# Optimization experiments

Hardware: AMD Instinct MI355X
Metric: run time of the kernel (lower is better)

## Reference

```python
import jax, jax.numpy as jnp
import numpy as np

B, C, H, W = 16, 512, 32, 32
HW = H * W  # == input_features == output_features for shapes to be consistent


def setup_inputs() -> dict:
    key = jax.random.key(0)
    k1, k2, k3 = jax.random.split(key, 3)
    node1 = jax.random.normal(k1, (B, C, H, W), dtype=jnp.float32)
    node2 = jax.random.normal(k2, (B, C, H, W), dtype=jnp.float32)
    # nn.Linear(input_features, output_features, bias=False).weight: [out, in]
    W_c = jax.random.normal(k3, (HW, HW), dtype=jnp.float32) * (1.0 / np.sqrt(HW))
    return {"node1": node1, "node2": node2, "W_c": W_c}


def reference(node1, node2, W_c):
    b, c, h, w = node1.shape
    hw = h * w
    n1 = node1.reshape(b, c, hw)  # [B, C, HW]
    n2 = node2.reshape(b, c, hw)  # [B, C, HW]
    # x = W_c(n1): Linear applies y = x @ W^T  -> [B, C, HW_out]
    x = jnp.einsum('bch,oh->bco', n1, W_c)
    # e = bmm(x.permute(0,2,1), n2): [B, HW_out, C] @ [B, C, HW] -> [B, HW_out, HW]
    e = jnp.einsum('bco,bch->boh', x, n2)
    a = jax.nn.softmax(e, axis=-1)  # softmax over last dim (HW of node2)
    # m = bmm(n2, a): [B, C, HW] @ [B, HW, HW] -> [B, C, HW]
    m = jnp.einsum('bck,bkj->bcj', n2, a)
    return m
```

## Files before the change

### kernel.cpp

```cpp
#include <hip/hip_runtime.h>
#include <math.h>


typedef _Float16 f16;
typedef _Float16 f16x8 __attribute__((ext_vector_type(8)));
typedef _Float16 f16x4 __attribute__((ext_vector_type(4)));
typedef float f32x4 __attribute__((ext_vector_type(4)));

__device__ __forceinline__ void glds16(const void* g, void* l) {
    __builtin_amdgcn_global_load_lds((const __attribute__((address_space(1))) void*)g,
                                     (__attribute__((address_space(3))) void*)l, 16, 0, 0);
}

__global__ __launch_bounds__(256) void prep(const float* __restrict__ n1,
                                            const float* __restrict__ Wc,
                                            const float* __restrict__ n2,
                                            f16* __restrict__ n1f, f16* __restrict__ Wf,
                                            f16* __restrict__ n2f, f16* __restrict__ n2t) {
    const int bid = blockIdx.x, tid = threadIdx.x;
    if (bid < 4608) {
        const float* s = (bid < 4096) ? n1 : Wc;
        f16* d = (bid < 4096) ? n1f : Wf;
        const size_t i = ((size_t)(bid < 4096 ? bid : bid - 4096) * 256 + tid) * 8;
        f32x4 a = *(const f32x4*)(s + i);
        f32x4 b = *(const f32x4*)(s + i + 4);
        f16x8 o;
        o[0] = (f16)a[0]; o[1] = (f16)a[1]; o[2] = (f16)a[2]; o[3] = (f16)a[3];
        o[4] = (f16)b[0]; o[5] = (f16)b[1]; o[6] = (f16)b[2]; o[7] = (f16)b[3];
        *(f16x8*)(d + i) = o;
        return;
    }
    const int id = bid - 4608;
    const int b = id >> 7;
    const int ry = (id & 127) >> 4;
    const int cx = id & 15;
    const float* S = n2 + (size_t)b * 512 * 1024;
    f16* Dn = n2f + (size_t)b * 512 * 1024;
    f16* Dt = n2t + (size_t)b * 1024 * 512;
    __shared__ f16 Ts[64 * 72];
    const int r0 = ry * 64, c0 = cx * 64;
    const int rr = tid >> 3, cc8 = (tid & 7) * 8;
#pragma unroll
    for (int h = 0; h < 2; ++h) {
        const int row = r0 + rr + 32 * h;
        const float* s = S + (size_t)row * 1024 + c0 + cc8;
        f32x4 a = *(const f32x4*)s, bq = *(const f32x4*)(s + 4);
        f16x8 o;
        o[0] = (f16)a[0]; o[1] = (f16)a[1]; o[2] = (f16)a[2]; o[3] = (f16)a[3];
        o[4] = (f16)bq[0]; o[5] = (f16)bq[1]; o[6] = (f16)bq[2]; o[7] = (f16)bq[3];
        *(f16x8*)&Ts[(rr + 32 * h) * 72 + cc8] = o;
        *(f16x8*)(Dn + (size_t)row * 1024 + c0 + cc8) = o;
    }
    __syncthreads();
    const int j = tid >> 2, k16 = (tid & 3) * 16;
    f16* d = Dt + (size_t)(c0 + j) * 512 + r0 + k16;
    f16x8 o0, o1;
#pragma unroll
    for (int i = 0; i < 8; ++i) {
        o0[i] = Ts[(k16 + i) * 72 + j];
        o1[i] = Ts[(k16 + 8 + i) * 72 + j];
    }
    *(f16x8*)d = o0;
    *(f16x8*)(d + 8) = o1;
}

__global__ __launch_bounds__(256) void softmax_stats(const f16* __restrict__ E,
                                                     float* __restrict__ Mg,
                                                     float* __restrict__ Si) {
    const int wave = threadIdx.x >> 6, lane = threadIdx.x & 63;
    const int row = blockIdx.x * 4 + wave;
    const f16* p = E + (size_t)row * 1024 + lane * 16;
    f16x8 a = *(const f16x8*)p, b = *(const f16x8*)(p + 8);
    float v[16];
#pragma unroll
    for (int i = 0; i < 8; ++i) { v[i] = (float)a[i]; v[i + 8] = (float)b[i]; }
    float m = v[0];
#pragma unroll
    for (int i = 1; i < 16; ++i) m = fmaxf(m, v[i]);
#pragma unroll
    for (int off = 1; off < 64; off <<= 1) m = fmaxf(m, __shfl_xor(m, off, 64));
    float s = 0.f;
#pragma unroll
    for (int i = 0; i < 16; ++i) s += __expf(v[i] - m);
#pragma unroll
    for (int off = 1; off < 64; off <<= 1) s += __shfl_xor(s, off, 64);
    if (lane == 0) { Mg[row] = m; Si[row] = 1.0f / s; }
}

__global__ __launch_bounds__(256) void tr_scale(const f16* __restrict__ S,
                                                const float* __restrict__ Mg,
                                                const float* __restrict__ Si,
                                                f16* __restrict__ D) {
    const int b = blockIdx.z;
    S += (size_t)b * 1024 * 1024;
    D += (size_t)b * 1024 * 1024;
    __shared__ f16 Ts[64 * 72];
    const int r0 = blockIdx.y * 64, c0 = blockIdx.x * 64;
    const int tid = threadIdx.x;
    const int rr = tid >> 3, cc8 = (tid & 7) * 8;
#pragma unroll
    for (int h = 0; h < 2; ++h) {
        const int row = r0 + rr + 32 * h;
        const float mg = Mg[b * 1024 + row];
        const float si = Si[b * 1024 + row];
        f16x8 v = *(const f16x8*)(S + (size_t)row * 1024 + c0 + cc8);
        f16x8 o;
#pragma unroll
        for (int i = 0; i < 8; ++i) o[i] = (f16)(__expf((float)v[i] - mg) * si);
        *(f16x8*)&Ts[(rr + 32 * h) * 72 + cc8] = o;
    }
    __syncthreads();
    const int j = tid >> 2, k16 = (tid & 3) * 16;
    f16* d = D + (size_t)(c0 + j) * 1024 + r0 + k16;
    f16x8 o0, o1;
#pragma unroll
    for (int i = 0; i < 8; ++i) {
        o0[i] = Ts[(k16 + i) * 72 + j];
        o1[i] = Ts[(k16 + 8 + i) * 72 + j];
    }
    *(f16x8*)d = o0;
    *(f16x8*)(d + 8) = o1;
}

__global__ __launch_bounds__(512) void gemm1_nt_xt(const f16* __restrict__ A,
                                                   const f16* __restrict__ Bw,
                                                   f16* __restrict__ Xt) {
    const int M = 512, K = 1024;
    const int id = blockIdx.x;
    const int xcd = id & 7, loc = id >> 3;
    const int b = xcd * 2 + (loc >> 5);
    const int m0 = ((loc >> 3) & 3) * 128;
    const int n0 = (loc & 7) * 128;
    A += (size_t)b * M * K;
    Xt += (size_t)b * 1024 * M;
    __shared__ __attribute__((aligned(16))) f16 SM[128 * 136];
    f16* As = SM;
    f16* Bs = SM + 4096;
    const int tid = threadIdx.x, lane = tid & 63, wave = tid >> 6;
    const int col = lane & 15, quad = lane >> 4;
    const int wm = (wave & 1) * 64, wn = (wave >> 1) * 32;
    const int off = wave * 1024 + lane * 16;
    const char* gA = (const char*)(A + (size_t)(m0 + (off >> 6)) * K) + (off & 63);
    const char* gB = (const char*)(Bw + (size_t)(n0 + (off >> 6)) * K) + (off & 63);
    char* lA = (char*)As + wave * 1024;
    char* lB = (char*)Bs + wave * 1024;

    f32x4 acc[4][2] = {};
    for (int kb = 0; kb < K * 2; kb += 64) {
        glds16(gA + kb, lA);
        glds16(gB + kb, lB);
        __syncthreads();
        f16x8 fa[4], fb[2];
#pragma unroll
        for (int u = 0; u < 4; ++u) fa[u] = *(const f16x8*)&As[(wm + u * 16 + col) * 32 + quad * 8];
#pragma unroll
        for (int v = 0; v < 2; ++v) fb[v] = *(const f16x8*)&Bs[(wn + v * 16 + col) * 32 + quad * 8];
#pragma unroll
        for (int u = 0; u < 4; ++u)
#pragma unroll
            for (int v = 0; v < 2; ++v)
                acc[u][v] = __builtin_amdgcn_mfma_f32_16x16x32_f16(fa[u], fb[v], acc[u][v], 0, 0, 0);
        __syncthreads();
    }
    f16* Tt = SM;
#pragma unroll
    for (int u = 0; u < 4; ++u)
#pragma unroll
        for (int v = 0; v < 2; ++v) {
            f16x4 p;
#pragma unroll
            for (int r = 0; r < 4; ++r) p[r] = (f16)acc[u][v][r];
            *(f16x4*)&Tt[(wn + v * 16 + col) * 136 + wm + u * 16 + quad * 4] = p;
        }
    __syncthreads();
    const int j = tid >> 2, seg = (tid & 3) * 32;
    f16* dst = Xt + (size_t)(n0 + j) * M + m0 + seg;
#pragma unroll
    for (int c8 = 0; c8 < 32; c8 += 8)
        *(f16x8*)(dst + c8) = *(const f16x8*)&Tt[j * 136 + seg + c8];
}

__global__ __launch_bounds__(512) void gemm2_nt_e(const f16* __restrict__ A,
                                                  const f16* __restrict__ B,
                                                  f16* __restrict__ E) {
    const int K = 512;
    const int id = blockIdx.x;
    const int xcd = id & 7, loc = id >> 3;
    const int b = xcd * 2 + (loc >> 6);
    const int m0 = ((loc >> 3) & 7) * 128;
    const int n0 = (loc & 7) * 128;
    A += (size_t)b * 1024 * K;
    B += (size_t)b * 1024 * K;
    E += (size_t)b * 1024 * 1024;
    __shared__ __attribute__((aligned(16))) f16 As[128 * 32], Bs[128 * 32];
    const int tid = threadIdx.x, lane = tid & 63, wave = tid >> 6;
    const int col = lane & 15, quad = lane >> 4;
    const int wm = (wave & 1) * 64, wn = (wave >> 1) * 32;
    const int off = wave * 1024 + lane * 16;
    const char* gA = (const char*)(A + (size_t)(m0 + (off >> 6)) * K) + (off & 63);
    const char* gB = (const char*)(B + (size_t)(n0 + (off >> 6)) * K) + (off & 63);
    char* lA = (char*)As + wave * 1024;
    char* lB = (char*)Bs + wave * 1024;

    f32x4 acc[4][2] = {};
    for (int kb = 0; kb < K * 2; kb += 64) {
        glds16(gA + kb, lA);
        glds16(gB + kb, lB);
        __syncthreads();
        f16x8 fa[4], fb[2];
#pragma unroll
        for (int u = 0; u < 4; ++u) fa[u] = *(const f16x8*)&As[(wm + u * 16 + col) * 32 + quad * 8];
#pragma unroll
        for (int v = 0; v < 2; ++v) fb[v] = *(const f16x8*)&Bs[(wn + v * 16 + col) * 32 + quad * 8];
#pragma unroll
        for (int u = 0; u < 4; ++u)
#pragma unroll
            for (int v = 0; v < 2; ++v)
                acc[u][v] = __builtin_amdgcn_mfma_f32_16x16x32_f16(fa[u], fb[v], acc[u][v], 0, 0, 0);
        __syncthreads();
    }
#pragma unroll
    for (int u = 0; u < 4; ++u)
#pragma unroll
        for (int v = 0; v < 2; ++v)
#pragma unroll
            for (int r = 0; r < 4; ++r)
                E[(size_t)(m0 + wm + u * 16 + quad * 4 + r) * 1024 + n0 + wn + v * 16 + col] =
                    (f16)acc[u][v][r];
}

__global__ __launch_bounds__(512) void gemm3_nt_out(const f16* __restrict__ A,
                                                    const f16* __restrict__ Bt,
                                                    float* __restrict__ C) {
    const int K = 1024;
    const int id = blockIdx.x;
    const int xcd = id & 7, loc = id >> 3;
    const int b = xcd * 2 + (loc >> 5);
    const int m0 = ((loc >> 3) & 3) * 128;
    const int n0 = (loc & 7) * 128;
    A += (size_t)b * 512 * K;
    Bt += (size_t)b * 1024 * K;
    C += (size_t)b * 512 * 1024;
    __shared__ __attribute__((aligned(16))) f16 As[128 * 32], Bs[128 * 32];
    const int tid = threadIdx.x, lane = tid & 63, wave = tid >> 6;
    const int col = lane & 15, quad = lane >> 4;
    const int wm = (wave & 1) * 64, wn = (wave >> 1) * 32;
    const int off = wave * 1024 + lane * 16;
    const char* gA = (const char*)(A + (size_t)(m0 + (off >> 6)) * K) + (off & 63);
    const char* gB = (const char*)(Bt + (size_t)(n0 + (off >> 6)) * K) + (off & 63);
    char* lA = (char*)As + wave * 1024;
    char* lB = (char*)Bs + wave * 1024;

    f32x4 acc[4][2] = {};
    for (int kb = 0; kb < K * 2; kb += 64) {
        glds16(gA + kb, lA);
        glds16(gB + kb, lB);
        __syncthreads();
        f16x8 fa[4], fb[2];
#pragma unroll
        for (int u = 0; u < 4; ++u) fa[u] = *(const f16x8*)&As[(wm + u * 16 + col) * 32 + quad * 8];
#pragma unroll
        for (int v = 0; v < 2; ++v) fb[v] = *(const f16x8*)&Bs[(wn + v * 16 + col) * 32 + quad * 8];
#pragma unroll
        for (int u = 0; u < 4; ++u)
#pragma unroll
            for (int v = 0; v < 2; ++v)
                acc[u][v] = __builtin_amdgcn_mfma_f32_16x16x32_f16(fa[u], fb[v], acc[u][v], 0, 0, 0);
        __syncthreads();
    }
#pragma unroll
    for (int u = 0; u < 4; ++u)
#pragma unroll
        for (int v = 0; v < 2; ++v)
#pragma unroll
            for (int r = 0; r < 4; ++r)
                C[(size_t)(m0 + wm + u * 16 + quad * 4 + r) * 1024 + n0 + wn + v * 16 + col] =
                    acc[u][v][r];
}

extern "C" void kernel_launch(void* const* d_in, const int* in_sizes, int n_in,
                              void* d_out, int out_size, void* d_ws, size_t ws_size,
                              hipStream_t stream) {
    const float* n1 = (const float*)d_in[0];
    const float* n2 = (const float*)d_in[1];
    const float* Wc = (const float*)d_in[2];
    float* out = (float*)d_out;
    char* ws = (char*)d_ws;

    f16* n2t = (f16*)(ws);
    f16* Xt  = (f16*)(ws + (16u << 20));
    f16* Wf  = (f16*)(ws + (32u << 20));
    f16* E   = (f16*)(ws + (32u << 20));
    f16* n1f = (f16*)(ws + (64u << 20));
    f16* n2f = (f16*)(ws + (80u << 20));
    float* Mg = (float*)(ws + (64u << 20));
    float* Si = (float*)(ws + (64u << 20) + (1u << 16));
    f16* At  = (f16*)(ws);

    prep<<<6656, dim3(256), 0, stream>>>(n1, Wc, n2, n1f, Wf, n2f, n2t);
    gemm1_nt_xt<<<512, dim3(512), 0, stream>>>(n1f, Wf, Xt);
    gemm2_nt_e<<<1024, dim3(512), 0, stream>>>(Xt, n2t, E);
    softmax_stats<<<4096, dim3(256), 0, stream>>>(E, Mg, Si);
    tr_scale<<<dim3(16, 16, 16), dim3(256), 0, stream>>>(E, Mg, Si, At);
    gemm3_nt_out<<<512, dim3(512), 0, stream>>>(n2f, At, out);
}
```

Baseline: 213.8 us.

## Double-buffer GEMM LDS tiles with register prefetch and one barrier per step

Replaces the direct global-to-LDS loads in the three GEMM kernels with a shared macro. It prefetches the next K-slice into registers and writes it into a second LDS buffer while MFMAs run on the current one. This cuts the per-iteration barriers from two to one and overlaps global load latency with compute. In exchange it doubles LDS use per block, adds register pressure, and fully unrolls the K loop, which may lower occupancy or enlarge code size.

```diff
diff --git a/kernel.cpp b/kernel.cpp
--- a/kernel.cpp
+++ b/kernel.cpp
@@ -7,10 +7,7 @@
 typedef _Float16 f16x4 __attribute__((ext_vector_type(4)));
 typedef float f32x4 __attribute__((ext_vector_type(4)));
 
-__device__ __forceinline__ void glds16(const void* g, void* l) {
-    __builtin_amdgcn_global_load_lds((const __attribute__((address_space(1))) void*)g,
-                                     (__attribute__((address_space(3))) void*)l, 16, 0, 0);
-}
+#define WG_BARRIER() asm volatile("s_waitcnt lgkmcnt(0)\ns_barrier" ::: "memory")
 
 __global__ __launch_bounds__(256) void prep(const float* __restrict__ n1,
                                             const float* __restrict__ Wc,
@@ -122,6 +119,42 @@
     *(f16x8*)(d + 8) = o1;
 }
 
+#define GEMM_CORE(NS)                                                                   \
+    f16x8 ra = *(const f16x8*)gAp, rb = *(const f16x8*)gBp;                             \
+    *(f16x8*)wA0 = ra; *(f16x8*)wB0 = rb;                                               \
+    ra = *(const f16x8*)(gAp + 64); rb = *(const f16x8*)(gBp + 64);                     \
+    WG_BARRIER();                                                                       \
+    f32x4 acc[4][2] = {};                                                               \
+_Pragma("unroll")                                                                       \
+    for (int kb = 0; kb < (NS); ++kb) {                                                 \
+        const f16* Ac = (const f16*)(SM + (kb & 1) * 8192);                             \
+        const f16* Bc = (const f16*)(SM + 16384 + (kb & 1) * 8192);                     \
+        f16x8 fa[4], fb[2];                                                             \
+_Pragma("unroll")                                                                       \
+        for (int u = 0; u < 4; ++u)                                                     \
+            fa[u] = *(const f16x8*)&Ac[(wm + u * 16 + col) * 32 + quad * 8];            \
+_Pragma("unroll")                                                                       \
+        for (int v = 0; v < 2; ++v)                                                     \
+            fb[v] = *(const f16x8*)&Bc[(wn + v * 16 + col) * 32 + quad * 8];            \
+_Pragma("unroll")                                                                       \
+        for (int u = 0; u < 4; ++u)                                                     \
+_Pragma("unroll")                                                                       \
+            for (int v = 0; v < 2; ++v)                                                 \
+                acc[u][v] = __builtin_amdgcn_mfma_f32_16x16x32_f16(fa[u], fb[v],        \
+                                                                   acc[u][v], 0, 0, 0);\
+        if (kb + 1 < (NS)) {                                                            \
+            char* dA = SM + ((kb + 1) & 1) * 8192 + off;                                \
+            char* dB = SM + 16384 + ((kb + 1) & 1) * 8192 + off;                        \
+            *(f16x8*)dA = ra;                                                           \
+            *(f16x8*)dB = rb;                                                           \
+            if (kb + 2 < (NS)) {                                                        \
+                ra = *(const f16x8*)(gAp + (size_t)(kb + 2) * 64);                      \
+                rb = *(const f16x8*)(gBp + (size_t)(kb + 2) * 64);                      \
+            }                                                                           \
+            WG_BARRIER();                                                               \
+        }                                                                               \
+    }
+
 __global__ __launch_bounds__(512) void gemm1_nt_xt(const f16* __restrict__ A,
                                                    const f16* __restrict__ Bw,
                                                    f16* __restrict__ Xt) {
@@ -133,36 +166,21 @@
     const int n0 = (loc & 7) * 128;
     A += (size_t)b * M * K;
     Xt += (size_t)b * 1024 * M;
-    __shared__ __attribute__((aligned(16))) f16 SM[128 * 136];
-    f16* As = SM;
-    f16* Bs = SM + 4096;
+    __shared__ __attribute__((aligned(16))) char SM[34816];
     const int tid = threadIdx.x, lane = tid & 63, wave = tid >> 6;
     const int col = lane & 15, quad = lane >> 4;
     const int wm = (wave & 1) * 64, wn = (wave >> 1) * 32;
     const int off = wave * 1024 + lane * 16;
-    const char* gA = (const char*)(A + (size_t)(m0 + (off >> 6)) * K) + (off & 63);
-    const char* gB = (const char*)(Bw + (size_t)(n0 + (off >> 6)) * K) + (off & 63);
-    char* lA = (char*)As + wave * 1024;
-    char* lB = (char*)Bs + wave * 1024;
-
-    f32x4 acc[4][2] = {};
-    for (int kb = 0; kb < K * 2; kb += 64) {
-        glds16(gA + kb, lA);
-        glds16(gB + kb, lB);
-        __syncthreads();
-        f16x8 fa[4], fb[2];
-#pragma unroll
-        for (int u = 0; u < 4; ++u) fa[u] = *(const f16x8*)&As[(wm + u * 16 + col) * 32 + quad * 8];
-#pragma unroll
-        for (int v = 0; v < 2; ++v) fb[v] = *(const f16x8*)&Bs[(wn + v * 16 + col) * 32 + quad * 8];
-#pragma unroll
-        for (int u = 0; u < 4; ++u)
-#pragma unroll
-            for (int v = 0; v < 2; ++v)
-                acc[u][v] = __builtin_amdgcn_mfma_f32_16x16x32_f16(fa[u], fb[v], acc[u][v], 0, 0, 0);
-        __syncthreads();
-    }
-    f16* Tt = SM;
+    const int srow = off >> 6, scolb = off & 63;
+    const char* gAp = (const char*)A + (size_t)(m0 + srow) * K * 2 + scolb;
+    const char* gBp = (const char*)Bw + (size_t)(n0 + srow) * K * 2 + scolb;
+    char* wA0 = SM + off;
+    char* wB0 = SM + 16384 + off;
+
+    GEMM_CORE(32)
+
+    WG_BARRIER();
+    f16* Tt = (f16*)SM;
 #pragma unroll
     for (int u = 0; u < 4; ++u)
 #pragma unroll
@@ -172,7 +190,7 @@
             for (int r = 0; r < 4; ++r) p[r] = (f16)acc[u][v][r];
             *(f16x4*)&Tt[(wn + v * 16 + col) * 136 + wm + u * 16 + quad * 4] = p;
         }
-    __syncthreads();
+    WG_BARRIER();
     const int j = tid >> 2, seg = (tid & 3) * 32;
     f16* dst = Xt + (size_t)(n0 + j) * M + m0 + seg;
 #pragma unroll
@@ -192,33 +210,19 @@
     A += (size_t)b * 1024 * K;
     B += (size_t)b * 1024 * K;
     E += (size_t)b * 1024 * 1024;
-    __shared__ __attribute__((aligned(16))) f16 As[128 * 32], Bs[128 * 32];
+    __shared__ __attribute__((aligned(16))) char SM[32768];
     const int tid = threadIdx.x, lane = tid & 63, wave = tid >> 6;
     const int col = lane & 15, quad = lane >> 4;
     const int wm = (wave & 1) * 64, wn = (wave >> 1) * 32;
     const int off = wave * 1024 + lane * 16;
-    const char* gA = (const char*)(A + (size_t)(m0 + (off >> 6)) * K) + (off & 63);
-    const char* gB = (const char*)(B + (size_t)(n0 + (off >> 6)) * K) + (off & 63);
-    char* lA = (char*)As + wave * 1024;
-    char* lB = (char*)Bs + wave * 1024;
-
-    f32x4 acc[4][2] = {};
-    for (int kb = 0; kb < K * 2; kb += 64) {
-        glds16(gA + kb, lA);
-        glds16(gB + kb, lB);
-        __syncthreads();
-        f16x8 fa[4], fb[2];
-#pragma unroll
-        for (int u = 0; u < 4; ++u) fa[u] = *(const f16x8*)&As[(wm + u * 16 + col) * 32 + quad * 8];
-#pragma unroll
-        for (int v = 0; v < 2; ++v) fb[v] = *(const f16x8*)&Bs[(wn + v * 16 + col) * 32 + quad * 8];
-#pragma unroll
-        for (int u = 0; u < 4; ++u)
-#pragma unroll
-            for (int v = 0; v < 2; ++v)
-                acc[u][v] = __builtin_amdgcn_mfma_f32_16x16x32_f16(fa[u], fb[v], acc[u][v], 0, 0, 0);
-        __syncthreads();
-    }
+    const int srow = off >> 6, scolb = off & 63;
+    const char* gAp = (const char*)A + (size_t)(m0 + srow) * K * 2 + scolb;
+    const char* gBp = (const char*)B + (size_t)(n0 + srow) * K * 2 + scolb;
+    char* wA0 = SM + off;
+    char* wB0 = SM + 16384 + off;
+
+    GEMM_CORE(16)
+
 #pragma unroll
     for (int u = 0; u < 4; ++u)
 #pragma unroll
@@ -241,33 +245,19 @@
     A += (size_t)b * 512 * K;
     Bt += (size_t)b * 1024 * K;
     C += (size_t)b * 512 * 1024;
-    __shared__ __attribute__((aligned(16))) f16 As[128 * 32], Bs[128 * 32];
+    __shared__ __attribute__((aligned(16))) char SM[32768];
     const int tid = threadIdx.x, lane = tid & 63, wave = tid >> 6;
     const int col = lane & 15, quad = lane >> 4;
     const int wm = (wave & 1) * 64, wn = (wave >> 1) * 32;
     const int off = wave * 1024 + lane * 16;
-    const char* gA = (const char*)(A + (size_t)(m0 + (off >> 6)) * K) + (off & 63);
-    const char* gB = (const char*)(Bt + (size_t)(n0 + (off >> 6)) * K) + (off & 63);
-    char* lA = (char*)As + wave * 1024;
-    char* lB = (char*)Bs + wave * 1024;
-
-    f32x4 acc[4][2] = {};
-    for (int kb = 0; kb < K * 2; kb += 64) {
-        glds16(gA + kb, lA);
-        glds16(gB + kb, lB);
-        __syncthreads();
-        f16x8 fa[4], fb[2];
-#pragma unroll
-        for (int u = 0; u < 4; ++u) fa[u] = *(const f16x8*)&As[(wm + u * 16 + col) * 32 + quad * 8];
-#pragma unroll
-        for (int v = 0; v < 2; ++v) fb[v] = *(const f16x8*)&Bs[(wn + v * 16 + col) * 32 + quad * 8];
-#pragma unroll
-        for (int u = 0; u < 4; ++u)
-#pragma unroll
-            for (int v = 0; v < 2; ++v)
-                acc[u][v] = __builtin_amdgcn_mfma_f32_16x16x32_f16(fa[u], fb[v], acc[u][v], 0, 0, 0);
-        __syncthreads();
-    }
+    const int srow = off >> 6, scolb = off & 63;
+    const char* gAp = (const char*)A + (size_t)(m0 + srow) * K * 2 + scolb;
+    const char* gBp = (const char*)Bt + (size_t)(n0 + srow) * K * 2 + scolb;
+    char* wA0 = SM + off;
+    char* wB0 = SM + 16384 + off;
+
+    GEMM_CORE(32)
+
 #pragma unroll
     for (int u = 0; u < 4; ++u)
 #pragma unroll
```

After: 203.6 us. 1.05x faster.
